# Optimization experiments

Measured on AMD Instinct MI355X. Metric: run time of the kernel, lower is better.

Reference implementation:

```python
import jax, jax.numpy as jnp
import numpy as np

H = 20  # hidden_size

def _lstm_layer(x_tbf, w_ih, w_hh, b_ih, b_hh):
    # x_tbf: [T, B, F]; torch gate order: i, f, g, o
    T, B, _ = x_tbf.shape
    # precompute input projections once: [T, B, 4H]
    xproj = jnp.einsum('tbf,gf->tbg', x_tbf, w_ih) + b_ih + b_hh

    def step(carry, xp_t):
        h, c = carry
        gates = xp_t + h @ w_hh.T  # [B, 4H]
        i, f, g, o = jnp.split(gates, 4, axis=-1)
        i = jax.nn.sigmoid(i)
        f = jax.nn.sigmoid(f)
        g = jnp.tanh(g)
        o = jax.nn.sigmoid(o)
        c = f * c + i * g
        h = o * jnp.tanh(c)
        return (h, c), h

    h0 = jnp.zeros((B, H), dtype=x_tbf.dtype)
    c0 = jnp.zeros((B, H), dtype=x_tbf.dtype)
    (_, _), hs = jax.lax.scan(step, (h0, c0), xproj)
    return hs  # [T, B, H]

def setup_inputs() -> dict:
    key = jax.random.key(0)
    ks = jax.random.split(key, 11)
    F_in = 10
    s_ih0 = 1.0 / np.sqrt(H)
    inp = {
        'x': jax.random.normal(ks[0], (4096, 512, F_in), dtype=jnp.float32),
        'w_ih0': jax.random.uniform(ks[1], (4 * H, F_in), minval=-s_ih0, maxval=s_ih0),
        'w_hh0': jax.random.uniform(ks[2], (4 * H, H), minval=-s_ih0, maxval=s_ih0),
        'b_ih0': jax.random.uniform(ks[3], (4 * H,), minval=-s_ih0, maxval=s_ih0),
        'b_hh0': jax.random.uniform(ks[4], (4 * H,), minval=-s_ih0, maxval=s_ih0),
        'w_ih1': jax.random.uniform(ks[5], (4 * H, H), minval=-s_ih0, maxval=s_ih0),
        'w_hh1': jax.random.uniform(ks[6], (4 * H, H), minval=-s_ih0, maxval=s_ih0),
        'b_ih1': jax.random.uniform(ks[7], (4 * H,), minval=-s_ih0, maxval=s_ih0),
        'b_hh1': jax.random.uniform(ks[8], (4 * H,), minval=-s_ih0, maxval=s_ih0),
        'w_fc': jax.random.uniform(ks[9], (1, H), minval=-s_ih0, maxval=s_ih0),
        'b_fc': jax.random.uniform(ks[10], (1,), minval=-s_ih0, maxval=s_ih0),
    }
    return inp

def reference(x, w_ih0, w_hh0, b_ih0, b_hh0, w_ih1, w_hh1, b_ih1, b_hh1, w_fc, b_fc):
    # x: [B, T, F] (batch_first) -> [T, B, F] for scan
    x_tbf = jnp.swapaxes(x, 0, 1)
    h1 = _lstm_layer(x_tbf, w_ih0, w_hh0, b_ih0, b_hh0)  # [T, B, H]
    h2 = _lstm_layer(h1, w_ih1, w_hh1, b_ih1, b_hh1)     # [T, B, H]
    last = h2[-1]                                          # [B, H]
    return last @ w_fc.T + b_fc                            # [B, 1]
```

## Files before the change

### kernel.cpp

```cpp
#include <hip/hip_runtime.h>

#define T_STEPS 512
#define HS 20
#define F0 10
#define BPB 6
#define NB_TOT 4096
#define NBLK ((NB_TOT + BPB - 1) / BPB)

__device__ __forceinline__ float sigmoid_fast(float v) {
    return __fdividef(1.f, 1.f + __expf(-v));
}
__device__ __forceinline__ float tanh_fast(float v) {
    return 1.f - __fdividef(2.f, __expf(2.f * v) + 1.f);
}
#define PIN(v) asm volatile("" : "+v"(v))

__global__ __launch_bounds__(128, 2)
void lstm2_fc_kernel(const float* __restrict__ x,
                     const float* __restrict__ wih0, const float* __restrict__ whh0,
                     const float* __restrict__ bih0, const float* __restrict__ bhh0,
                     const float* __restrict__ wih1, const float* __restrict__ whh1,
                     const float* __restrict__ bih1, const float* __restrict__ bhh1,
                     const float* __restrict__ wfc,  const float* __restrict__ bfc,
                     float* __restrict__ out)
{
    const int tid  = threadIdx.x;
    const int wid  = tid >> 6;
    const int lane = tid & 63;
    const int g    = (lane / HS) % 3;
    const int u    = lane % HS;
    const int bgA  = blockIdx.x * BPB + g;
    const int bgBr = blockIdx.x * BPB + g + 3;
    const bool okB = (bgBr < NB_TOT);
    const int bgB  = okB ? bgBr : (NB_TOT - 1);

    __shared__ float s_h0[2][BPB][HS];
    __shared__ float s_h1[BPB][HS];

    for (int i = tid; i < 2 * BPB * HS; i += 128) (&s_h0[0][0][0])[i] = 0.f;
    for (int i = tid; i < BPB * HS; i += 128)     (&s_h1[0][0])[i]    = 0.f;

    float w[4][2 * HS], bias[4];
    if (wid == 0) {
        #pragma unroll
        for (int q = 0; q < 4; ++q) {
            const int row = q * HS + u;
            #pragma unroll
            for (int f = 0; f < F0; ++f) { w[q][f] = wih0[row * F0 + f]; PIN(w[q][f]); }
            #pragma unroll
            for (int j = 0; j < HS; ++j) { w[q][F0 + j] = whh0[row * HS + j]; PIN(w[q][F0 + j]); }
            bias[q] = bih0[row] + bhh0[row]; PIN(bias[q]);
        }
    } else {
        #pragma unroll
        for (int q = 0; q < 4; ++q) {
            const int row = q * HS + u;
            #pragma unroll
            for (int j = 0; j < HS; ++j) { w[q][j]      = wih1[row * HS + j]; PIN(w[q][j]); }
            #pragma unroll
            for (int j = 0; j < HS; ++j) { w[q][HS + j] = whh1[row * HS + j]; PIN(w[q][HS + j]); }
            bias[q] = bih1[row] + bhh1[row]; PIN(bias[q]);
        }
    }

    float cA = 0.f, cB = 0.f;
    const float* xbA = x + (size_t)bgA * (T_STEPS * F0);
    const float* xbB = x + (size_t)bgB * (T_STEPS * F0);

    __syncthreads();

    for (int t = 0; t <= T_STEPS; ++t) {
        if (wid == 0) {
            if (t < T_STEPS) {
                float xA[F0], xB[F0];
                {
                    const float2* pA = (const float2*)(xbA + t * F0);
                    const float2* pB = (const float2*)(xbB + t * F0);
                    #pragma unroll
                    for (int f = 0; f < F0 / 2; ++f) {
                        float2 vA = pA[f], vB = pB[f];
                        xA[2*f] = vA.x; xA[2*f+1] = vA.y;
                        xB[2*f] = vB.x; xB[2*f+1] = vB.y;
                    }
                }
                float aA0 = bias[0], aA1 = bias[1], aA2 = bias[2], aA3 = bias[3];
                float aB0 = bias[0], aB1 = bias[1], aB2 = bias[2], aB3 = bias[3];
                const float* hpA = &s_h0[(t + 1) & 1][g][0];
                const float* hpB = &s_h0[(t + 1) & 1][g + 3][0];
                #pragma unroll
                for (int q4 = 0; q4 < HS / 4; ++q4) {
                    const float4 hA = *(const float4*)(hpA + 4 * q4);
                    const float4 hB = *(const float4*)(hpB + 4 * q4);
                    const float eA[4] = {hA.x, hA.y, hA.z, hA.w};
                    const float eB[4] = {hB.x, hB.y, hB.z, hB.w};
                    #pragma unroll
                    for (int s = 0; s < 4; ++s) {
                        const int k = F0 + 4 * q4 + s;
                        aA0 = fmaf(eA[s], w[0][k], aA0);  aB0 = fmaf(eB[s], w[0][k], aB0);
                        aA1 = fmaf(eA[s], w[1][k], aA1);  aB1 = fmaf(eB[s], w[1][k], aB1);
                        aA2 = fmaf(eA[s], w[2][k], aA2);  aB2 = fmaf(eB[s], w[2][k], aB2);
                        aA3 = fmaf(eA[s], w[3][k], aA3);  aB3 = fmaf(eB[s], w[3][k], aB3);
                    }
                }
                #pragma unroll
                for (int f = 0; f < F0; ++f) {
                    aA0 = fmaf(xA[f], w[0][f], aA0);  aB0 = fmaf(xB[f], w[0][f], aB0);
                    aA1 = fmaf(xA[f], w[1][f], aA1);  aB1 = fmaf(xB[f], w[1][f], aB1);
                    aA2 = fmaf(xA[f], w[2][f], aA2);  aB2 = fmaf(xB[f], w[2][f], aB2);
                    aA3 = fmaf(xA[f], w[3][f], aA3);  aB3 = fmaf(xB[f], w[3][f], aB3);
                }
                {
                    const float iA = sigmoid_fast(aA0), fA = sigmoid_fast(aA1);
                    const float gA = tanh_fast(aA2),    oA = sigmoid_fast(aA3);
                    cA = fA * cA + iA * gA;
                    s_h0[t & 1][g][u] = oA * tanh_fast(cA);
                    const float iB = sigmoid_fast(aB0), fB = sigmoid_fast(aB1);
                    const float fgB = tanh_fast(aB2),   oB = sigmoid_fast(aB3);
                    cB = fB * cB + iB * fgB;
                    s_h0[t & 1][g + 3][u] = oB * tanh_fast(cB);
                }
            }
        } else {
            if (t >= 1) {
                float aA0 = bias[0], aA1 = bias[1], aA2 = bias[2], aA3 = bias[3];
                float aB0 = bias[0], aB1 = bias[1], aB2 = bias[2], aB3 = bias[3];
                const float* hpA = &s_h0[(t - 1) & 1][g][0];
                const float* hpB = &s_h0[(t - 1) & 1][g + 3][0];
                #pragma unroll
                for (int q4 = 0; q4 < HS / 4; ++q4) {
                    const float4 hA = *(const float4*)(hpA + 4 * q4);
                    const float4 hB = *(const float4*)(hpB + 4 * q4);
                    const float eA[4] = {hA.x, hA.y, hA.z, hA.w};
                    const float eB[4] = {hB.x, hB.y, hB.z, hB.w};
                    #pragma unroll
                    for (int s = 0; s < 4; ++s) {
                        const int k = 4 * q4 + s;
                        aA0 = fmaf(eA[s], w[0][k], aA0);  aB0 = fmaf(eB[s], w[0][k], aB0);
                        aA1 = fmaf(eA[s], w[1][k], aA1);  aB1 = fmaf(eB[s], w[1][k], aB1);
                        aA2 = fmaf(eA[s], w[2][k], aA2);  aB2 = fmaf(eB[s], w[2][k], aB2);
                        aA3 = fmaf(eA[s], w[3][k], aA3);  aB3 = fmaf(eB[s], w[3][k], aB3);
                    }
                }
                const float* ppA = &s_h1[g][0];
                const float* ppB = &s_h1[g + 3][0];
                #pragma unroll
                for (int q4 = 0; q4 < HS / 4; ++q4) {
                    const float4 hA = *(const float4*)(ppA + 4 * q4);
                    const float4 hB = *(const float4*)(ppB + 4 * q4);
                    const float eA[4] = {hA.x, hA.y, hA.z, hA.w};
                    const float eB[4] = {hB.x, hB.y, hB.z, hB.w};
                    #pragma unroll
                    for (int s = 0; s < 4; ++s) {
                        const int k = HS + 4 * q4 + s;
                        aA0 = fmaf(eA[s], w[0][k], aA0);  aB0 = fmaf(eB[s], w[0][k], aB0);
                        aA1 = fmaf(eA[s], w[1][k], aA1);  aB1 = fmaf(eB[s], w[1][k], aB1);
                        aA2 = fmaf(eA[s], w[2][k], aA2);  aB2 = fmaf(eB[s], w[2][k], aB2);
                        aA3 = fmaf(eA[s], w[3][k], aA3);  aB3 = fmaf(eB[s], w[3][k], aB3);
                    }
                }
                const float iA = sigmoid_fast(aA0), fA = sigmoid_fast(aA1);
                const float gA = tanh_fast(aA2),    oA = sigmoid_fast(aA3);
                const float iB = sigmoid_fast(aB0), fB = sigmoid_fast(aB1);
                const float gB = tanh_fast(aB2),    oB = sigmoid_fast(aB3);
                cA = fA * cA + iA * gA;
                cB = fB * cB + iB * gB;
                __builtin_amdgcn_wave_barrier();
                s_h1[g][u]     = oA * tanh_fast(cA);
                s_h1[g + 3][u] = oB * tanh_fast(cB);
            }
        }
        __syncthreads();
    }

    if (wid == 1 && lane < 60 && u == 0) {
        float oA = bfc[0], oB = bfc[0];
        #pragma unroll
        for (int j = 0; j < HS; ++j) {
            oA = fmaf(s_h1[g][j],     wfc[j], oA);
            oB = fmaf(s_h1[g + 3][j], wfc[j], oB);
        }
        out[bgA] = oA;
        if (okB) out[bgBr] = oB;
    }
}

extern "C" void kernel_launch(void* const* d_in, const int* in_sizes, int n_in,
                              void* d_out, int out_size, void* d_ws, size_t ws_size,
                              hipStream_t stream) {
    const float* x    = (const float*)d_in[0];
    const float* wih0 = (const float*)d_in[1];
    const float* whh0 = (const float*)d_in[2];
    const float* bih0 = (const float*)d_in[3];
    const float* bhh0 = (const float*)d_in[4];
    const float* wih1 = (const float*)d_in[5];
    const float* whh1 = (const float*)d_in[6];
    const float* bih1 = (const float*)d_in[7];
    const float* bhh1 = (const float*)d_in[8];
    const float* wfc  = (const float*)d_in[9];
    const float* bfc  = (const float*)d_in[10];
    float* out = (float*)d_out;

    dim3 grid(NBLK), block(128);
    hipLaunchKernelGGL(lstm2_fc_kernel, grid, block, 0, stream,
                       x, wih0, whh0, bih0, bhh0,
                       wih1, whh1, bih1, bhh1, wfc, bfc, out);
}
```

Measured before the change: 909.5 us.

## Chunk layer pipeline into 32-step blocks and prefetch next input step

Layer 0 and layer 1 waves now exchange hidden states through a double-buffered chunk of 32 timesteps in shared memory, so the block-wide barrier runs once per chunk instead of once per timestep, with layer 1 lagging by one chunk. The input x for the next step is loaded into registers before the current step's recurrent math, hiding global load latency. Each wave relies on in-wave ordering of LDS writes and reads inside a chunk, and shared memory per block grows, which may affect occupancy.

```diff
diff --git a/kernel.cpp b/kernel.cpp
--- a/kernel.cpp
+++ b/kernel.cpp
@@ -6,6 +6,8 @@
 #define BPB 6
 #define NB_TOT 4096
 #define NBLK ((NB_TOT + BPB - 1) / BPB)
+#define CHK 32
+#define NCH (T_STEPS / CHK)
 
 __device__ __forceinline__ float sigmoid_fast(float v) {
     return __fdividef(1.f, 1.f + __expf(-v));
@@ -34,11 +36,13 @@
     const bool okB = (bgBr < NB_TOT);
     const int bgB  = okB ? bgBr : (NB_TOT - 1);
 
-    __shared__ float s_h0[2][BPB][HS];
+    __shared__ float buf[2][CHK][BPB][HS];
     __shared__ float s_h1[BPB][HS];
 
-    for (int i = tid; i < 2 * BPB * HS; i += 128) (&s_h0[0][0][0])[i] = 0.f;
-    for (int i = tid; i < BPB * HS; i += 128)     (&s_h1[0][0])[i]    = 0.f;
+    for (int i = tid; i < BPB * HS; i += 128) {
+        (&s_h1[0][0])[i]            = 0.f;
+        (&buf[1][CHK - 1][0][0])[i] = 0.f;
+    }
 
     float w[4][2 * HS], bias[4];
     if (wid == 0) {
@@ -67,26 +71,48 @@
     const float* xbA = x + (size_t)bgA * (T_STEPS * F0);
     const float* xbB = x + (size_t)bgB * (T_STEPS * F0);
 
+    float2 xnA[F0 / 2], xnB[F0 / 2];
+    if (wid == 0) {
+        const float2* pA = (const float2*)xbA;
+        const float2* pB = (const float2*)xbB;
+        #pragma unroll
+        for (int f2 = 0; f2 < F0 / 2; ++f2) { xnA[f2] = pA[f2]; xnB[f2] = pB[f2]; }
+    }
+
     __syncthreads();
 
-    for (int t = 0; t <= T_STEPS; ++t) {
-        if (wid == 0) {
-            if (t < T_STEPS) {
-                float xA[F0], xB[F0];
-                {
-                    const float2* pA = (const float2*)(xbA + t * F0);
-                    const float2* pB = (const float2*)(xbB + t * F0);
-                    #pragma unroll
-                    for (int f = 0; f < F0 / 2; ++f) {
-                        float2 vA = pA[f], vB = pB[f];
-                        xA[2*f] = vA.x; xA[2*f+1] = vA.y;
-                        xB[2*f] = vB.x; xB[2*f+1] = vB.y;
-                    }
-                }
+    for (int k = 0; k <= NCH; ++k) {
+        if (wid == 0 && k < NCH) {
+            float* wb = &buf[k & 1][0][0][0];
+            const float* hprev_c = &buf[(k + 1) & 1][CHK - 1][0][0];
+            #pragma unroll 1
+            for (int s = 0; s < CHK; ++s) {
+                const int t = k * CHK + s;
                 float aA0 = bias[0], aA1 = bias[1], aA2 = bias[2], aA3 = bias[3];
                 float aB0 = bias[0], aB1 = bias[1], aB2 = bias[2], aB3 = bias[3];
-                const float* hpA = &s_h0[(t + 1) & 1][g][0];
-                const float* hpB = &s_h0[(t + 1) & 1][g + 3][0];
+                #pragma unroll
+                for (int f2 = 0; f2 < F0 / 2; ++f2) {
+                    const int f = 2 * f2;
+                    const float2 vA = xnA[f2], vB = xnB[f2];
+                    aA0 = fmaf(vA.x, w[0][f], aA0); aA0 = fmaf(vA.y, w[0][f + 1], aA0);
+                    aA1 = fmaf(vA.x, w[1][f], aA1); aA1 = fmaf(vA.y, w[1][f + 1], aA1);
+                    aA2 = fmaf(vA.x, w[2][f], aA2); aA2 = fmaf(vA.y, w[2][f + 1], aA2);
+                    aA3 = fmaf(vA.x, w[3][f], aA3); aA3 = fmaf(vA.y, w[3][f + 1], aA3);
+                    aB0 = fmaf(vB.x, w[0][f], aB0); aB0 = fmaf(vB.y, w[0][f + 1], aB0);
+                    aB1 = fmaf(vB.x, w[1][f], aB1); aB1 = fmaf(vB.y, w[1][f + 1], aB1);
+                    aB2 = fmaf(vB.x, w[2][f], aB2); aB2 = fmaf(vB.y, w[2][f + 1], aB2);
+                    aB3 = fmaf(vB.x, w[3][f], aB3); aB3 = fmaf(vB.y, w[3][f + 1], aB3);
+                }
+                {
+                    const int tn = (t + 1 < T_STEPS) ? (t + 1) : (T_STEPS - 1);
+                    const float2* pA = (const float2*)(xbA + tn * F0);
+                    const float2* pB = (const float2*)(xbB + tn * F0);
+                    #pragma unroll
+                    for (int f2 = 0; f2 < F0 / 2; ++f2) { xnA[f2] = pA[f2]; xnB[f2] = pB[f2]; }
+                }
+                const float* hb  = (s > 0) ? (wb + (s - 1) * (BPB * HS)) : hprev_c;
+                const float* hpA = hb + g * HS;
+                const float* hpB = hb + (g + 3) * HS;
                 #pragma unroll
                 for (int q4 = 0; q4 < HS / 4; ++q4) {
                     const float4 hA = *(const float4*)(hpA + 4 * q4);
@@ -94,38 +120,34 @@
                     const float eA[4] = {hA.x, hA.y, hA.z, hA.w};
                     const float eB[4] = {hB.x, hB.y, hB.z, hB.w};
                     #pragma unroll
-                    for (int s = 0; s < 4; ++s) {
-                        const int k = F0 + 4 * q4 + s;
-                        aA0 = fmaf(eA[s], w[0][k], aA0);  aB0 = fmaf(eB[s], w[0][k], aB0);
-                        aA1 = fmaf(eA[s], w[1][k], aA1);  aB1 = fmaf(eB[s], w[1][k], aB1);
-                        aA2 = fmaf(eA[s], w[2][k], aA2);  aB2 = fmaf(eB[s], w[2][k], aB2);
-                        aA3 = fmaf(eA[s], w[3][k], aA3);  aB3 = fmaf(eB[s], w[3][k], aB3);
+                    for (int e = 0; e < 4; ++e) {
+                        const int kk = F0 + 4 * q4 + e;
+                        aA0 = fmaf(eA[e], w[0][kk], aA0);  aB0 = fmaf(eB[e], w[0][kk], aB0);
+                        aA1 = fmaf(eA[e], w[1][kk], aA1);  aB1 = fmaf(eB[e], w[1][kk], aB1);
+                        aA2 = fmaf(eA[e], w[2][kk], aA2);  aB2 = fmaf(eB[e], w[2][kk], aB2);
+                        aA3 = fmaf(eA[e], w[3][kk], aA3);  aB3 = fmaf(eB[e], w[3][kk], aB3);
                     }
                 }
-                #pragma unroll
-                for (int f = 0; f < F0; ++f) {
-                    aA0 = fmaf(xA[f], w[0][f], aA0);  aB0 = fmaf(xB[f], w[0][f], aB0);
-                    aA1 = fmaf(xA[f], w[1][f], aA1);  aB1 = fmaf(xB[f], w[1][f], aB1);
-                    aA2 = fmaf(xA[f], w[2][f], aA2);  aB2 = fmaf(xB[f], w[2][f], aB2);
-                    aA3 = fmaf(xA[f], w[3][f], aA3);  aB3 = fmaf(xB[f], w[3][f], aB3);
-                }
-                {
-                    const float iA = sigmoid_fast(aA0), fA = sigmoid_fast(aA1);
-                    const float gA = tanh_fast(aA2),    oA = sigmoid_fast(aA3);
-                    cA = fA * cA + iA * gA;
-                    s_h0[t & 1][g][u] = oA * tanh_fast(cA);
-                    const float iB = sigmoid_fast(aB0), fB = sigmoid_fast(aB1);
-                    const float fgB = tanh_fast(aB2),   oB = sigmoid_fast(aB3);
-                    cB = fB * cB + iB * fgB;
-                    s_h0[t & 1][g + 3][u] = oB * tanh_fast(cB);
-                }
+                const float iA = sigmoid_fast(aA0), fA = sigmoid_fast(aA1);
+                const float gA = tanh_fast(aA2),    oA = sigmoid_fast(aA3);
+                cA = fA * cA + iA * gA;
+                const float hAo = oA * tanh_fast(cA);
+                const float iB = sigmoid_fast(aB0), fB = sigmoid_fast(aB1);
+                const float gB = tanh_fast(aB2),    oB = sigmoid_fast(aB3);
+                cB = fB * cB + iB * gB;
+                const float hBo = oB * tanh_fast(cB);
+                float* wr = wb + s * (BPB * HS);
+                wr[g * HS + u]       = hAo;
+                wr[(g + 3) * HS + u] = hBo;
             }
-        } else {
-            if (t >= 1) {
+        } else if (wid == 1 && k >= 1) {
+            const float* rb = &buf[(k - 1) & 1][0][0][0];
+            #pragma unroll 1
+            for (int s = 0; s < CHK; ++s) {
                 float aA0 = bias[0], aA1 = bias[1], aA2 = bias[2], aA3 = bias[3];
                 float aB0 = bias[0], aB1 = bias[1], aB2 = bias[2], aB3 = bias[3];
-                const float* hpA = &s_h0[(t - 1) & 1][g][0];
-                const float* hpB = &s_h0[(t - 1) & 1][g + 3][0];
+                const float* hpA = rb + s * (BPB * HS) + g * HS;
+                const float* hpB = rb + s * (BPB * HS) + (g + 3) * HS;
                 #pragma unroll
                 for (int q4 = 0; q4 < HS / 4; ++q4) {
                     const float4 hA = *(const float4*)(hpA + 4 * q4);
@@ -133,12 +155,12 @@
                     const float eA[4] = {hA.x, hA.y, hA.z, hA.w};
                     const float eB[4] = {hB.x, hB.y, hB.z, hB.w};
                     #pragma unroll
-                    for (int s = 0; s < 4; ++s) {
-                        const int k = 4 * q4 + s;
-                        aA0 = fmaf(eA[s], w[0][k], aA0);  aB0 = fmaf(eB[s], w[0][k], aB0);
-                        aA1 = fmaf(eA[s], w[1][k], aA1);  aB1 = fmaf(eB[s], w[1][k], aB1);
-                        aA2 = fmaf(eA[s], w[2][k], aA2);  aB2 = fmaf(eB[s], w[2][k], aB2);
-                        aA3 = fmaf(eA[s], w[3][k], aA3);  aB3 = fmaf(eB[s], w[3][k], aB3);
+                    for (int e = 0; e < 4; ++e) {
+                        const int kk = 4 * q4 + e;
+                        aA0 = fmaf(eA[e], w[0][kk], aA0);  aB0 = fmaf(eB[e], w[0][kk], aB0);
+                        aA1 = fmaf(eA[e], w[1][kk], aA1);  aB1 = fmaf(eB[e], w[1][kk], aB1);
+                        aA2 = fmaf(eA[e], w[2][kk], aA2);  aB2 = fmaf(eB[e], w[2][kk], aB2);
+                        aA3 = fmaf(eA[e], w[3][kk], aA3);  aB3 = fmaf(eB[e], w[3][kk], aB3);
                     }
                 }
                 const float* ppA = &s_h1[g][0];
@@ -150,12 +172,12 @@
                     const float eA[4] = {hA.x, hA.y, hA.z, hA.w};
                     const float eB[4] = {hB.x, hB.y, hB.z, hB.w};
                     #pragma unroll
-                    for (int s = 0; s < 4; ++s) {
-                        const int k = HS + 4 * q4 + s;
-                        aA0 = fmaf(eA[s], w[0][k], aA0);  aB0 = fmaf(eB[s], w[0][k], aB0);
-                        aA1 = fmaf(eA[s], w[1][k], aA1);  aB1 = fmaf(eB[s], w[1][k], aB1);
-                        aA2 = fmaf(eA[s], w[2][k], aA2);  aB2 = fmaf(eB[s], w[2][k], aB2);
-                        aA3 = fmaf(eA[s], w[3][k], aA3);  aB3 = fmaf(eB[s], w[3][k], aB3);
+                    for (int e = 0; e < 4; ++e) {
+                        const int kk = HS + 4 * q4 + e;
+                        aA0 = fmaf(eA[e], w[0][kk], aA0);  aB0 = fmaf(eB[e], w[0][kk], aB0);
+                        aA1 = fmaf(eA[e], w[1][kk], aA1);  aB1 = fmaf(eB[e], w[1][kk], aB1);
+                        aA2 = fmaf(eA[e], w[2][kk], aA2);  aB2 = fmaf(eB[e], w[2][kk], aB2);
+                        aA3 = fmaf(eA[e], w[3][kk], aA3);  aB3 = fmaf(eB[e], w[3][kk], aB3);
                     }
                 }
                 const float iA = sigmoid_fast(aA0), fA = sigmoid_fast(aA1);
```

Result: no change. 897.6 us (-1.3%).

## Split LSTM gates across two waves per layer with shared-memory exchange

Applied to the files above, without the earlier changes.

Each layer now uses two wavefronts instead of one, each computing two of the four gates, which halves per-thread FMA work and weight registers. The gate values are exchanged through shared memory and combined by one wave, at the cost of a second __syncthreads per timestep. Layer-1 hidden state becomes double-buffered, and the layer-0 input for the next step is prefetched into registers to hide global load latency. The block grows to 256 threads, with launch bounds changed to allow three blocks per unit.

```diff
diff --git a/kernel.cpp b/kernel.cpp
--- a/kernel.cpp
+++ b/kernel.cpp
@@ -15,7 +15,7 @@
 }
 #define PIN(v) asm volatile("" : "+v"(v))
 
-__global__ __launch_bounds__(128, 2)
+__global__ __launch_bounds__(256, 3)
 void lstm2_fc_kernel(const float* __restrict__ x,
                      const float* __restrict__ wih0, const float* __restrict__ whh0,
                      const float* __restrict__ bih0, const float* __restrict__ bhh0,
@@ -24,42 +24,49 @@
                      const float* __restrict__ wfc,  const float* __restrict__ bfc,
                      float* __restrict__ out)
 {
-    const int tid  = threadIdx.x;
-    const int wid  = tid >> 6;
-    const int lane = tid & 63;
-    const int g    = (lane / HS) % 3;
-    const int u    = lane % HS;
-    const int bgA  = blockIdx.x * BPB + g;
-    const int bgBr = blockIdx.x * BPB + g + 3;
-    const bool okB = (bgBr < NB_TOT);
-    const int bgB  = okB ? bgBr : (NB_TOT - 1);
+    const int tid   = threadIdx.x;
+    const int wid   = tid >> 6;
+    const int lane  = tid & 63;
+    const int g     = (lane / HS) % 3;
+    const int u     = lane % HS;
+    const int layer = wid >> 1;
+    const int half  = wid & 1;
+    const int q0    = 2 * half;
+    const int bgA   = blockIdx.x * BPB + g;
+    const int bgBr  = blockIdx.x * BPB + g + 3;
+    const bool okB  = (bgBr < NB_TOT);
+    const int bgB   = okB ? bgBr : (NB_TOT - 1);
 
     __shared__ float s_h0[2][BPB][HS];
-    __shared__ float s_h1[BPB][HS];
-
-    for (int i = tid; i < 2 * BPB * HS; i += 128) (&s_h0[0][0][0])[i] = 0.f;
-    for (int i = tid; i < BPB * HS; i += 128)     (&s_h1[0][0])[i]    = 0.f;
-
-    float w[4][2 * HS], bias[4];
-    if (wid == 0) {
-        #pragma unroll
-        for (int q = 0; q < 4; ++q) {
-            const int row = q * HS + u;
-            #pragma unroll
-            for (int f = 0; f < F0; ++f) { w[q][f] = wih0[row * F0 + f]; PIN(w[q][f]); }
-            #pragma unroll
-            for (int j = 0; j < HS; ++j) { w[q][F0 + j] = whh0[row * HS + j]; PIN(w[q][F0 + j]); }
-            bias[q] = bih0[row] + bhh0[row]; PIN(bias[q]);
+    __shared__ float s_h1[2][BPB][HS];
+    __shared__ float ex0[BPB][HS][2];
+    __shared__ float ex1[BPB][HS][2];
+
+    for (int i = tid; i < 2 * BPB * HS; i += 256) {
+        (&s_h0[0][0][0])[i] = 0.f;
+        (&s_h1[0][0][0])[i] = 0.f;
+    }
+
+    float w[2][2 * HS], bias[2];
+    if (layer == 0) {
+        #pragma unroll
+        for (int qh = 0; qh < 2; ++qh) {
+            const int row = (q0 + qh) * HS + u;
+            #pragma unroll
+            for (int f = 0; f < F0; ++f) { w[qh][f] = wih0[row * F0 + f]; PIN(w[qh][f]); }
+            #pragma unroll
+            for (int j = 0; j < HS; ++j) { w[qh][F0 + j] = whh0[row * HS + j]; PIN(w[qh][F0 + j]); }
+            bias[qh] = bih0[row] + bhh0[row]; PIN(bias[qh]);
         }
     } else {
         #pragma unroll
-        for (int q = 0; q < 4; ++q) {
-            const int row = q * HS + u;
-            #pragma unroll
-            for (int j = 0; j < HS; ++j) { w[q][j]      = wih1[row * HS + j]; PIN(w[q][j]); }
-            #pragma unroll
-            for (int j = 0; j < HS; ++j) { w[q][HS + j] = whh1[row * HS + j]; PIN(w[q][HS + j]); }
-            bias[q] = bih1[row] + bhh1[row]; PIN(bias[q]);
+        for (int qh = 0; qh < 2; ++qh) {
+            const int row = (q0 + qh) * HS + u;
+            #pragma unroll
+            for (int j = 0; j < HS; ++j) { w[qh][j]      = wih1[row * HS + j]; PIN(w[qh][j]); }
+            #pragma unroll
+            for (int j = 0; j < HS; ++j) { w[qh][HS + j] = whh1[row * HS + j]; PIN(w[qh][HS + j]); }
+            bias[qh] = bih1[row] + bhh1[row]; PIN(bias[qh]);
         }
     }
 
@@ -67,24 +74,40 @@
     const float* xbA = x + (size_t)bgA * (T_STEPS * F0);
     const float* xbB = x + (size_t)bgB * (T_STEPS * F0);
 
+    float2 xnA[F0 / 2], xnB[F0 / 2];
+    if (layer == 0) {
+        const float2* pA = (const float2*)xbA;
+        const float2* pB = (const float2*)xbB;
+        #pragma unroll
+        for (int f2 = 0; f2 < F0 / 2; ++f2) { xnA[f2] = pA[f2]; xnB[f2] = pB[f2]; }
+    }
+
     __syncthreads();
 
+    float tgA = 0.f, soA = 0.f, tgB = 0.f, soB = 0.f;
+
+    #pragma unroll 1
     for (int t = 0; t <= T_STEPS; ++t) {
-        if (wid == 0) {
+        if (layer == 0) {
             if (t < T_STEPS) {
-                float xA[F0], xB[F0];
+                float a0A = bias[0], a1A = bias[1];
+                float a0B = bias[0], a1B = bias[1];
+                #pragma unroll
+                for (int f2 = 0; f2 < F0 / 2; ++f2) {
+                    const int f = 2 * f2;
+                    const float2 vA = xnA[f2], vB = xnB[f2];
+                    a0A = fmaf(vA.x, w[0][f], a0A); a0A = fmaf(vA.y, w[0][f + 1], a0A);
+                    a1A = fmaf(vA.x, w[1][f], a1A); a1A = fmaf(vA.y, w[1][f + 1], a1A);
+                    a0B = fmaf(vB.x, w[0][f], a0B); a0B = fmaf(vB.y, w[0][f + 1], a0B);
+                    a1B = fmaf(vB.x, w[1][f], a1B); a1B = fmaf(vB.y, w[1][f + 1], a1B);
+                }
                 {
-                    const float2* pA = (const float2*)(xbA + t * F0);
-                    const float2* pB = (const float2*)(xbB + t * F0);
-                    #pragma unroll
-                    for (int f = 0; f < F0 / 2; ++f) {
-                        float2 vA = pA[f], vB = pB[f];
-                        xA[2*f] = vA.x; xA[2*f+1] = vA.y;
-                        xB[2*f] = vB.x; xB[2*f+1] = vB.y;
-                    }
-                }
-                float aA0 = bias[0], aA1 = bias[1], aA2 = bias[2], aA3 = bias[3];
-                float aB0 = bias[0], aB1 = bias[1], aB2 = bias[2], aB3 = bias[3];
+                    const int tn = (t + 1 < T_STEPS) ? (t + 1) : (T_STEPS - 1);
+                    const float2* pA = (const float2*)(xbA + tn * F0);
+                    const float2* pB = (const float2*)(xbB + tn * F0);
+                    #pragma unroll
+                    for (int f2 = 0; f2 < F0 / 2; ++f2) { xnA[f2] = pA[f2]; xnB[f2] = pB[f2]; }
+                }
                 const float* hpA = &s_h0[(t + 1) & 1][g][0];
                 const float* hpB = &s_h0[(t + 1) & 1][g + 3][0];
                 #pragma unroll
@@ -94,36 +117,24 @@
                     const float eA[4] = {hA.x, hA.y, hA.z, hA.w};
                     const float eB[4] = {hB.x, hB.y, hB.z, hB.w};
                     #pragma unroll
-                    for (int s = 0; s < 4; ++s) {
-                        const int k = F0 + 4 * q4 + s;
-                        aA0 = fmaf(eA[s], w[0][k], aA0);  aB0 = fmaf(eB[s], w[0][k], aB0);
-                        aA1 = fmaf(eA[s], w[1][k], aA1);  aB1 = fmaf(eB[s], w[1][k], aB1);
-                        aA2 = fmaf(eA[s], w[2][k], aA2);  aB2 = fmaf(eB[s], w[2][k], aB2);
-                        aA3 = fmaf(eA[s], w[3][k], aA3);  aB3 = fmaf(eB[s], w[3][k], aB3);
+                    for (int e = 0; e < 4; ++e) {
+                        const int k = F0 + 4 * q4 + e;
+                        a0A = fmaf(eA[e], w[0][k], a0A);  a0B = fmaf(eB[e], w[0][k], a0B);
+                        a1A = fmaf(eA[e], w[1][k], a1A);  a1B = fmaf(eB[e], w[1][k], a1B);
                     }
                 }
-                #pragma unroll
-                for (int f = 0; f < F0; ++f) {
-                    aA0 = fmaf(xA[f], w[0][f], aA0);  aB0 = fmaf(xB[f], w[0][f], aB0);
-                    aA1 = fmaf(xA[f], w[1][f], aA1);  aB1 = fmaf(xB[f], w[1][f], aB1);
-                    aA2 = fmaf(xA[f], w[2][f], aA2);  aB2 = fmaf(xB[f], w[2][f], aB2);
-                    aA3 = fmaf(xA[f], w[3][f], aA3);  aB3 = fmaf(xB[f], w[3][f], aB3);
-                }
-                {
-                    const float iA = sigmoid_fast(aA0), fA = sigmoid_fast(aA1);
-                    const float gA = tanh_fast(aA2),    oA = sigmoid_fast(aA3);
-                    cA = fA * cA + iA * gA;
-                    s_h0[t & 1][g][u] = oA * tanh_fast(cA);
-                    const float iB = sigmoid_fast(aB0), fB = sigmoid_fast(aB1);
-                    const float fgB = tanh_fast(aB2),   oB = sigmoid_fast(aB3);
-                    cB = fB * cB + iB * fgB;
-                    s_h0[t & 1][g + 3][u] = oB * tanh_fast(cB);
+                if (half == 0) {
+                    *(float2*)&ex0[g][u][0]     = make_float2(sigmoid_fast(a0A), sigmoid_fast(a1A));
+                    *(float2*)&ex0[g + 3][u][0] = make_float2(sigmoid_fast(a0B), sigmoid_fast(a1B));
+                } else {
+                    tgA = tanh_fast(a0A); soA = sigmoid_fast(a1A);
+                    tgB = tanh_fast(a0B); soB = sigmoid_fast(a1B);
                 }
             }
         } else {
             if (t >= 1) {
-                float aA0 = bias[0], aA1 = bias[1], aA2 = bias[2], aA3 = bias[3];
-                float aB0 = bias[0], aB1 = bias[1], aB2 = bias[2], aB3 = bias[3];
+                float a0A = bias[0], a1A = bias[1];
+                float a0B = bias[0], a1B = bias[1];
                 const float* hpA = &s_h0[(t - 1) & 1][g][0];
                 const float* hpB = &s_h0[(t - 1) & 1][g + 3][0];
                 #pragma unroll
@@ -133,16 +144,14 @@
                     const float eA[4] = {hA.x, hA.y, hA.z, hA.w};
                     const float eB[4] = {hB.x, hB.y, hB.z, hB.w};
                     #pragma unroll
-                    for (int s = 0; s < 4; ++s) {
-                        const int k = 4 * q4 + s;
-                        aA0 = fmaf(eA[s], w[0][k], aA0);  aB0 = fmaf(eB[s], w[0][k], aB0);
-                        aA1 = fmaf(eA[s], w[1][k], aA1);  aB1 = fmaf(eB[s], w[1][k], aB1);
-                        aA2 = fmaf(eA[s], w[2][k], aA2);  aB2 = fmaf(eB[s], w[2][k], aB2);
-                        aA3 = fmaf(eA[s], w[3][k], aA3);  aB3 = fmaf(eB[s], w[3][k], aB3);
+                    for (int e = 0; e < 4; ++e) {
+                        const int k = 4 * q4 + e;
+                        a0A = fmaf(eA[e], w[0][k], a0A);  a0B = fmaf(eB[e], w[0][k], a0B);
+                        a1A = fmaf(eA[e], w[1][k], a1A);  a1B = fmaf(eB[e], w[1][k], a1B);
                     }
                 }
-                const float* ppA = &s_h1[g][0];
-                const float* ppB = &s_h1[g + 3][0];
+                const float* ppA = &s_h1[t & 1][g][0];
+                const float* ppB = &s_h1[t & 1][g + 3][0];
                 #pragma unroll
                 for (int q4 = 0; q4 < HS / 4; ++q4) {
                     const float4 hA = *(const float4*)(ppA + 4 * q4);
@@ -150,34 +159,57 @@
                     const float eA[4] = {hA.x, hA.y, hA.z, hA.w};
                     const float eB[4] = {hB.x, hB.y, hB.z, hB.w};
                     #pragma unroll
-                    for (int s = 0; s < 4; ++s) {
-                        const int k = HS + 4 * q4 + s;
-                        aA0 = fmaf(eA[s], w[0][k], aA0);  aB0 = fmaf(eB[s], w[0][k], aB0);
-                        aA1 = fmaf(eA[s], w[1][k], aA1);  aB1 = fmaf(eB[s], w[1][k], aB1);
-                        aA2 = fmaf(eA[s], w[2][k], aA2);  aB2 = fmaf(eB[s], w[2][k], aB2);
-                        aA3 = fmaf(eA[s], w[3][k], aA3);  aB3 = fmaf(eB[s], w[3][k], aB3);
+                    for (int e = 0; e < 4; ++e) {
+                        const int k = HS + 4 * q4 + e;
+                        a0A = fmaf(eA[e], w[0][k], a0A);  a0B = fmaf(eB[e], w[0][k], a0B);
+                        a1A = fmaf(eA[e], w[1][k], a1A);  a1B = fmaf(eB[e], w[1][k], a1B);
                     }
                 }
-                const float iA = sigmoid_fast(aA0), fA = sigmoid_fast(aA1);
-                const float gA = tanh_fast(aA2),    oA = sigmoid_fast(aA3);
-                const float iB = sigmoid_fast(aB0), fB = sigmoid_fast(aB1);
-                const float gB = tanh_fast(aB2),    oB = sigmoid_fast(aB3);
-                cA = fA * cA + iA * gA;
-                cB = fB * cB + iB * gB;
-                __builtin_amdgcn_wave_barrier();
-                s_h1[g][u]     = oA * tanh_fast(cA);
-                s_h1[g + 3][u] = oB * tanh_fast(cB);
+                if (half == 0) {
+                    *(float2*)&ex1[g][u][0]     = make_float2(sigmoid_fast(a0A), sigmoid_fast(a1A));
+                    *(float2*)&ex1[g + 3][u][0] = make_float2(sigmoid_fast(a0B), sigmoid_fast(a1B));
+                } else {
+                    tgA = tanh_fast(a0A); soA = sigmoid_fast(a1A);
+                    tgB = tanh_fast(a0B); soB = sigmoid_fast(a1B);
+                }
             }
         }
         __syncthreads();
-    }
-
-    if (wid == 1 && lane < 60 && u == 0) {
+
+        if (half == 1) {
+            const bool act = (layer == 0) ? (t < T_STEPS) : (t >= 1);
+            if (act) {
+                float2 sifA, sifB;
+                if (layer == 0) {
+                    sifA = *(const float2*)&ex0[g][u][0];
+                    sifB = *(const float2*)&ex0[g + 3][u][0];
+                } else {
+                    sifA = *(const float2*)&ex1[g][u][0];
+                    sifB = *(const float2*)&ex1[g + 3][u][0];
+                }
+                cA = fmaf(sifA.y, cA, sifA.x * tgA);
+                cB = fmaf(sifB.y, cB, sifB.x * tgB);
+                const float hA = soA * tanh_fast(cA);
+                const float hB = soB * tanh_fast(cB);
+                if (layer == 0) {
+                    s_h0[t & 1][g][u]       = hA;
+                    s_h0[t & 1][g + 3][u]   = hB;
+                } else {
+                    s_h1[(t - 1) & 1][g][u]     = hA;
+                    s_h1[(t - 1) & 1][g + 3][u] = hB;
+                }
+            }
+        }
+        __syncthreads();
+    }
+
+    if (wid == 3 && lane < 60 && u == 0) {
+        const int sl = (T_STEPS - 1) & 1;
         float oA = bfc[0], oB = bfc[0];
         #pragma unroll
         for (int j = 0; j < HS; ++j) {
-            oA = fmaf(s_h1[g][j],     wfc[j], oA);
-            oB = fmaf(s_h1[g + 3][j], wfc[j], oB);
+            oA = fmaf(s_h1[sl][g][j],     wfc[j], oA);
+            oB = fmaf(s_h1[sl][g + 3][j], wfc[j], oB);
         }
         out[bgA] = oA;
         if (okB) out[bgBr] = oB;
@@ -200,7 +232,7 @@
     const float* bfc  = (const float*)d_in[10];
     float* out = (float*)d_out;
 
-    dim3 grid(NBLK), block(128);
+    dim3 grid(NBLK), block(256);
     hipLaunchKernelGGL(lstm2_fc_kernel, grid, block, 0, stream,
                        x, wih0, whh0, bih0, bhh0,
                        wih1, whh1, bih1, bhh1, wfc, bfc, out);
```

After: 749.5 us. 1.21x faster.
